# Performance work log

Measured on AMD Instinct MI355X. Metric: run time of the kernel, lower is better.

Reference implementation:

```python
import jax, jax.numpy as jnp
import numpy as np

N = 6000      # residues (nodes)
E = 120000    # edges (~20 neighbors per node)
D = 128       # node_embedding_dim
De = 128      # edge_embedding_dim
H = 4         # attention heads
L = 2         # encoder layers
C = 2 * D + De
NB, BMIN, BMAX = 16, 2.0, 22.0  # RBF params


def _ln(x, g, b):
    m = x.mean(-1, keepdims=True)
    v = ((x - m) ** 2).mean(-1, keepdims=True)
    return (x - m) / jnp.sqrt(v + 1e-5) * g + b


def setup_inputs() -> dict:
    key = jax.random.key(0)
    ks = iter(jax.random.split(key, 64))

    def nrm(shape, scale=0.05):
        return jax.random.normal(next(ks), shape, jnp.float32) * scale

    inp = {}
    inp['sequence_indices'] = jax.random.randint(next(ks), (N,), 0, 21)
    inp['edge_index'] = jax.random.randint(next(ks), (2, E), 0, N)
    inp['edge_distances'] = BMIN + (BMAX - BMIN) * jax.random.uniform(next(ks), (E,), jnp.float32)
    # parameters
    inp['seq_embed'] = nrm((21, D), 1.0)
    inp['edge_lin_W'] = nrm((NB, De)); inp['edge_lin_b'] = jnp.zeros((De,), jnp.float32)
    inp['aW_W'] = nrm((L, H, C, D)); inp['aW_b'] = jnp.zeros((L, H, D), jnp.float32)
    inp['aA_W'] = nrm((L, H, D));    inp['aA_b'] = jnp.zeros((L, H), jnp.float32)
    inp['nmlp_W1'] = nrm((L, C, D)); inp['nmlp_b1'] = jnp.zeros((L, D), jnp.float32)
    inp['nmlp_W2'] = nrm((L, D, D)); inp['nmlp_b2'] = jnp.zeros((L, D), jnp.float32)
    inp['nmlp_W3'] = nrm((L, D, D)); inp['nmlp_b3'] = jnp.zeros((L, D), jnp.float32)
    inp['dmlp_W1'] = nrm((L, D, 4 * D)); inp['dmlp_b1'] = jnp.zeros((L, 4 * D), jnp.float32)
    inp['dmlp_W2'] = nrm((L, 4 * D, D)); inp['dmlp_b2'] = jnp.zeros((L, D), jnp.float32)
    inp['emlp_W1'] = nrm((L, C, De));  inp['emlp_b1'] = jnp.zeros((L, De), jnp.float32)
    inp['emlp_W2'] = nrm((L, De, De)); inp['emlp_b2'] = jnp.zeros((L, De), jnp.float32)
    inp['emlp_W3'] = nrm((L, De, De)); inp['emlp_b3'] = jnp.zeros((L, De), jnp.float32)
    inp['aggr_W'] = nrm((L, H * D, D)); inp['aggr_b'] = jnp.zeros((L, D), jnp.float32)
    inp['n1_g'] = jnp.ones((L, D), jnp.float32);  inp['n1_b'] = jnp.zeros((L, D), jnp.float32)
    inp['e_g'] = jnp.ones((L, De), jnp.float32);  inp['e_b'] = jnp.zeros((L, De), jnp.float32)
    return inp


def reference(sequence_indices, edge_index, edge_distances, seq_embed,
              edge_lin_W, edge_lin_b, aW_W, aW_b, aA_W, aA_b,
              nmlp_W1, nmlp_b1, nmlp_W2, nmlp_b2, nmlp_W3, nmlp_b3,
              dmlp_W1, dmlp_b1, dmlp_W2, dmlp_b2,
              emlp_W1, emlp_b1, emlp_W2, emlp_b2, emlp_W3, emlp_b3,
              aggr_W, aggr_b, n1_g, n1_b, e_g, e_b):
    gelu = lambda x: jax.nn.gelu(x, approximate=False)  # torch default GELU is exact erf
    lrelu = lambda x: jnp.where(x > 0, x, 0.2 * x)      # LeakyReLU(0.2)

    nodes = seq_embed[sequence_indices]                  # [N, D]
    mu = jnp.linspace(BMIN, BMAX, NB)
    sig = (BMAX - BMIN) / NB
    rbf = jnp.exp(-(((edge_distances[:, None] - mu) / sig) ** 2)) + 1e-8  # [E, NB]
    eattr = rbf @ edge_lin_W + edge_lin_b                # [E, De]

    src, snk = edge_index[0], edge_index[1]
    n = nodes.shape[0]
    for l in range(L):
        feat = jnp.concatenate([nodes[src], nodes[snk], eattr], axis=1)        # [E, C]
        h = lrelu(jnp.einsum('ec,hcd->ehd', feat, aW_W[l]) + aW_b[l][None])    # [E, H, D]
        scores = jnp.einsum('ehd,hd->eh', h, aA_W[l]) + aA_b[l][None]          # [E, H]
        nupd = gelu(feat @ nmlp_W1[l] + nmlp_b1[l])
        nupd = gelu(nupd @ nmlp_W2[l] + nmlp_b2[l])
        nupd = nupd @ nmlp_W3[l] + nmlp_b3[l]                                   # [E, D]
        # scatter softmax over sink nodes (per head)
        smax = jax.ops.segment_max(scores, snk, num_segments=n)                 # [N, H]
        att = jnp.exp(scores - smax[snk])                                       # [E, H]
        norm = jax.ops.segment_sum(att + 1e-12, snk, num_segments=n)            # [N, H]
        att = att / norm[snk]
        msg = (att[:, :, None] * nupd[:, None, :]).reshape(E, H * D)            # head-major concat
        agg = jax.ops.segment_sum(msg, snk, num_segments=n)                     # [N, H*D]
        upd = agg @ aggr_W[l] + aggr_b[l]                                       # [N, D]
        nodes = _ln(nodes + upd, n1_g[l], n1_b[l])
        dense = gelu(nodes @ dmlp_W1[l] + dmlp_b1[l]) @ dmlp_W2[l] + dmlp_b2[l]
        # faithful to source: node_norm1 reused, residual re-adds attention update
        nodes = _ln(dense + upd, n1_g[l], n1_b[l])
        ef = jnp.concatenate([nodes[src], nodes[snk], eattr], axis=1)
        eu = gelu(ef @ emlp_W1[l] + emlp_b1[l])
        eu = gelu(eu @ emlp_W2[l] + emlp_b2[l])
        eu = eu @ emlp_W3[l] + emlp_b3[l]
        eattr = _ln(eattr + eu, e_g[l], e_b[l])
    return nodes, eattr
```

## Files before the change

### kernel.cpp

```cpp
#include <hip/hip_runtime.h>
#include <stdint.h>

#define NN 6000
#define EE 120000
#define DD 128
#define CC 384
#define HDIM 512
#define OUT_NODES (NN*DD)
#define OUT_TOTAL (NN*DD + EE*DD)
#define NODE_LO (NN*DD)
#define EDGE_LO (EE*DD)

typedef unsigned short u16;
typedef __bf16 bf16x8 __attribute__((ext_vector_type(8)));
typedef float f32x4 __attribute__((ext_vector_type(4)));

__device__ __forceinline__ float bf2f(u16 u){ union{unsigned i; float f;} x; x.i=(unsigned)u<<16; return x.f; }
__device__ __forceinline__ u16 f2bf(float f){ union{unsigned i; float f;} x; x.f=f; unsigned r=(x.i + 0x7fffu + ((x.i>>16)&1u))>>16; return (u16)r; }
__device__ __forceinline__ float gelu_f(float v){ return 0.5f*v*(1.f + erff(v*0.70710678118654752f)); }

__device__ __forceinline__ void stage16(void* l, const void* g) {
#if __has_builtin(__builtin_amdgcn_global_load_lds)
  __builtin_amdgcn_global_load_lds(
      (__attribute__((address_space(1))) void*)g,
      (__attribute__((address_space(3))) void*)l, 16, 0, 0);
#else
  *(uint4*)l = *(const uint4*)g;
#endif
}

__device__ __forceinline__ void mfma_step(const u16* buf, int wm, int wn, int lane,
                                          f32x4 acc[4][4])
{
  const int ml = lane & 15;
  const int qx = ((lane >> 4) ^ ((ml ^ (ml >> 2)) & 3)) & 3;
  bf16x8 a_h[4], a_l[4], v_h[4], v_l[4];
#pragma unroll
  for (int mi = 0; mi < 4; ++mi) {
    int ro = (wm*64 + mi*16 + ml)*32 + qx*8;
    a_h[mi] = *(const bf16x8*)(buf + ro);
    a_l[mi] = *(const bf16x8*)(buf + 4096 + ro);
  }
#pragma unroll
  for (int ni = 0; ni < 4; ++ni) {
    int ro = (wn*64 + ni*16 + ml)*32 + qx*8;
    v_h[ni] = *(const bf16x8*)(buf + 8192 + ro);
    v_l[ni] = *(const bf16x8*)(buf + 12288 + ro);
  }
#pragma unroll
  for (int mi = 0; mi < 4; ++mi)
#pragma unroll
    for (int ni = 0; ni < 4; ++ni) {
      acc[mi][ni] = __builtin_amdgcn_mfma_f32_16x16x32_bf16(a_h[mi], v_l[ni], acc[mi][ni], 0, 0, 0);
      acc[mi][ni] = __builtin_amdgcn_mfma_f32_16x16x32_bf16(a_l[mi], v_h[ni], acc[mi][ni], 0, 0, 0);
      acc[mi][ni] = __builtin_amdgcn_mfma_f32_16x16x32_bf16(a_h[mi], v_h[ni], acc[mi][ni], 0, 0, 0);
    }
}

__device__ __forceinline__ int xswz(int row, int col) {
  return row*128 + (col ^ ((row&3)<<3) ^ (((row>>2)&3)<<4));
}

__device__ __forceinline__ void mfma_stepX(const u16* X0, const u16* X1, const u16* BB,
                                           int t, int wm, int wn, int lane, f32x4 acc[4][4])
{
  const int ml = lane & 15, qq = lane >> 4;
  const int qx = (qq ^ ((ml ^ (ml >> 2)) & 3)) & 3;
  bf16x8 a_h[4], a_l[4], v_h[4], v_l[4];
#pragma unroll
  for (int mi = 0; mi < 4; ++mi) {
    int o = xswz(wm*64 + mi*16 + ml, t*32 + qq*8);
    a_h[mi] = *(const bf16x8*)(X0 + o);
    a_l[mi] = *(const bf16x8*)(X1 + o);
  }
#pragma unroll
  for (int ni = 0; ni < 4; ++ni) {
    int ro = (wn*64 + ni*16 + ml)*32 + qx*8;
    v_h[ni] = *(const bf16x8*)(BB + ro);
    v_l[ni] = *(const bf16x8*)(BB + 4096 + ro);
  }
#pragma unroll
  for (int mi = 0; mi < 4; ++mi)
#pragma unroll
    for (int ni = 0; ni < 4; ++ni) {
      acc[mi][ni] = __builtin_amdgcn_mfma_f32_16x16x32_bf16(a_h[mi], v_l[ni], acc[mi][ni], 0, 0, 0);
      acc[mi][ni] = __builtin_amdgcn_mfma_f32_16x16x32_bf16(a_l[mi], v_h[ni], acc[mi][ni], 0, 0, 0);
      acc[mi][ni] = __builtin_amdgcn_mfma_f32_16x16x32_bf16(a_h[mi], v_h[ni], acc[mi][ni], 0, 0, 0);
    }
}

__device__ __forceinline__ void coop_loadZ(
    float* ZT, const float* __restrict__ Zg, int zld, int zs0, int zn0,
    const int* __restrict__ src, const int* __restrict__ snk,
    int m0, int M, int tid)
{
#pragma unroll
  for (int it = 0; it < 16; ++it) {
    int idx = it*256 + tid;
    int row = idx >> 5, c4 = idx & 31;
    int gm = m0 + row; if (gm > M-1) gm = M-1;
    const float4 a4 = *((const float4*)(Zg + (size_t)src[gm]*zld + zs0) + c4);
    const float4 b4 = *((const float4*)(Zg + (size_t)snk[gm]*zld + zn0) + c4);
    float4 s4; s4.x = a4.x+b4.x; s4.y = a4.y+b4.y; s4.z = a4.z+b4.z; s4.w = a4.w+b4.w;
    int cs = (c4*4) ^ (((row>>2)&1)<<4);
    *(float4*)(ZT + row*128 + cs) = s4;
  }
}

__device__ __forceinline__ void scatter_X(f32x4 acc[4][4], const float* bias, int gelu_on,
                                          u16* X0, u16* X1, int tid)
{
  const int lane = tid & 63, cl = lane & 15, qr = (lane>>4)&3;
  const int wm = (tid>>6)&1, wn = (tid>>7)&1;
#pragma unroll
  for (int ni = 0; ni < 4; ++ni) {
    float bv = bias[wn*64 + ni*16 + cl];
#pragma unroll
    for (int mi = 0; mi < 4; ++mi)
#pragma unroll
      for (int rg = 0; rg < 4; ++rg) {
        int row = wm*64 + mi*16 + qr*4 + rg;
        int col = wn*64 + ni*16 + cl;
        float v = acc[mi][ni][rg] + bv;
        if (gelu_on) v = gelu_f(v);
        u16 h = f2bf(v);
        int o = xswz(row, col);
        X0[o] = h; X1[o] = f2bf(v - bf2f(h));
      }
  }
}

__device__ __forceinline__ void epilogue_f32(
    f32x4 acc[4][4], const float* bias, float* Cp, int M, int ldc,
    int m0, int n0, int tid)
{
  const int lane = tid & 63;
  const int wm = (tid>>6)&1, wn = (tid>>7)&1;
  const int rl = wm*64 + ((lane>>4)&3)*4;
  const int cl0 = wn*64 + (lane & 15);
#pragma unroll
  for (int ni = 0; ni < 4; ++ni) {
    int gn = n0 + cl0 + ni*16;
    float bv = bias ? bias[gn] : 0.f;
#pragma unroll
    for (int mi = 0; mi < 4; ++mi)
#pragma unroll
      for (int rg = 0; rg < 4; ++rg) {
        int gm = m0 + rl + mi*16 + rg;
        if (gm < M) Cp[(size_t)gm*ldc + gn] = acc[mi][ni][rg] + bv;
      }
  }
}

__device__ __forceinline__ void epilogue_hl(
    f32x4 acc[4][4], const float* bias, u16* Ch, u16* Cl, u16* SM,
    int M, int ldn, int gelu_on, int m0, int n0, int tid)
{
  const int lane = tid & 63, cl = lane & 15, qr = (lane>>4)&3;
  const int wm = (tid>>6)&1, wn = (tid>>7)&1;
#pragma unroll
  for (int ni = 0; ni < 4; ++ni) {
    float bv = bias[n0 + wn*64 + cl + ni*16];
#pragma unroll
    for (int mi = 0; mi < 4; ++mi)
#pragma unroll
      for (int rg = 0; rg < 4; ++rg) {
        float v = acc[mi][ni][rg] + bv;
        if (gelu_on) v = gelu_f(v);
        acc[mi][ni][rg] = v;
      }
  }
#pragma unroll
  for (int pass = 0; pass < 2; ++pass) {
#pragma unroll
    for (int mi = 0; mi < 4; ++mi)
#pragma unroll
      for (int ni = 0; ni < 4; ++ni)
#pragma unroll
        for (int rg = 0; rg < 4; ++rg) {
          int row = wm*64 + mi*16 + qr*4 + rg;
          int col = wn*64 + ni*16 + cl;
          float v = acc[mi][ni][rg];
          u16 h = f2bf(v);
          u16 w = pass ? f2bf(v - bf2f(h)) : h;
          SM[row*128 + (col ^ (qr<<4))] = w;
        }
    __syncthreads();
    u16* Cp = pass ? Cl : Ch;
#pragma unroll
    for (int it = 0; it < 8; ++it) {
      int idx = it*256 + tid;
      int row = idx >> 4, blk = idx & 15;
      uint4 val = *(const uint4*)(SM + row*128 + ((blk*8) ^ (((row>>2)&3)<<4)));
      int gm = m0 + row;
      if (gm < M) *(uint4*)(Cp + (size_t)gm*ldn + n0 + blk*8) = val;
    }
    __syncthreads();
  }
}

__global__ __launch_bounds__(256) void k_gemm2(
    const u16* A_h, const u16* A_l, int K,
    const u16* __restrict__ Bh, const u16* __restrict__ Bl,
    const float* __restrict__ bias, float* Cf,
    u16* Ch, u16* Cl, int M, int ldc, int epi)
{
  __shared__ __align__(16) u16 SM[2][16384];
  const int tid = threadIdx.x, lane = tid & 63;
  const int m0 = blockIdx.x*128, n0 = blockIdx.y*128;
  const int wm = (tid>>6)&1, wn = (tid>>7)&1;
  const u16* gA[2]; const u16* gAl[2]; const u16* gB[2]; const u16* gBl[2];
#pragma unroll
  for (int r = 0; r < 2; ++r) {
    int c = r*256 + tid, m = c>>2, q = c&3;
    int qs = q ^ ((m ^ (m>>2)) & 3);
    int gl = m0 + m; if (gl > M-1) gl = M-1;
    gA[r]  = A_h + (size_t)gl*K + qs*8;
    gAl[r] = A_l + (size_t)gl*K + qs*8;
    gB[r]  = Bh + (size_t)(n0+m)*K + qs*8;
    gBl[r] = Bl + (size_t)(n0+m)*K + qs*8;
  }
  auto stage = [&](int t, u16* buf) {
    int kt = t*32;
#pragma unroll
    for (int r = 0; r < 2; ++r) {
      int c8 = (r*256 + tid)*8;
      stage16(buf + c8,         gA[r]  + kt);
      stage16(buf + 4096 + c8,  gAl[r] + kt);
      stage16(buf + 8192 + c8,  gB[r]  + kt);
      stage16(buf + 12288 + c8, gBl[r] + kt);
    }
  };
  f32x4 acc[4][4] = {};
  const int nk = K >> 5;
  stage(0, SM[0]);
  for (int t = 0; t < nk; ++t) {
    __syncthreads();
    if (t + 1 < nk) stage(t + 1, SM[(t+1)&1]);
    mfma_step(SM[t&1], wm, wn, lane, acc);
  }
  __syncthreads();
  if (epi == 3) epilogue_f32(acc, bias, Cf, M, ldc, m0, n0, tid);
  else          epilogue_hl(acc, bias, Ch, Cl, SM[0], M, ldc, epi == 5, m0, n0, tid);
}

__global__ __launch_bounds__(256) void k_mlp_chain(
    const u16* __restrict__ nodes_h, const u16* __restrict__ eattr_h,
    const int* __restrict__ src, const int* __restrict__ snk,
    const u16* __restrict__ B1h, const u16* __restrict__ B1l, const float* __restrict__ b1,
    const u16* __restrict__ B2h, const u16* __restrict__ B2l, const float* __restrict__ b2,
    const u16* __restrict__ B3h, const u16* __restrict__ B3l, const float* __restrict__ b3,
    u16* __restrict__ Xh, u16* __restrict__ Xl, int M)
{
  __shared__ __align__(16) u16 SM[2][16384];
  __shared__ __align__(16) u16 BB[8192];
  const int tid = threadIdx.x, lane = tid & 63;
  const int m0 = blockIdx.x*128;
  const int wm = (tid>>6)&1, wn = (tid>>7)&1;
  const u16* pr0[2]; const u16* pr1[2]; const u16* pr2[2];
  const u16* gB[2]; const u16* gBl[2];
  int soff[2];
#pragma unroll
  for (int r = 0; r < 2; ++r) {
    int c = r*256 + tid, m = c>>2, q = c&3;
    int qs = q ^ ((m ^ (m>>2)) & 3);
    int gl = m0 + m; if (gl > M-1) gl = M-1;
    pr0[r] = nodes_h + (size_t)src[gl]*DD + qs*8;
    pr1[r] = nodes_h + (size_t)snk[gl]*DD + qs*8;
    pr2[r] = eattr_h + (size_t)gl*DD + qs*8;
    gB[r]  = B1h + (size_t)m*CC + qs*8;
    gBl[r] = B1l + (size_t)m*CC + qs*8;
    soff[r] = m*128 + qs*8;
  }
  auto stage_g = [&](int t, u16* buf) {
    int reg = t >> 2, kk = (t & 3) * 32;
    const int LO = (reg == 2) ? EDGE_LO : NODE_LO;
#pragma unroll
    for (int r = 0; r < 2; ++r) {
      int c8 = (r*256 + tid)*8;
      const u16* g = (reg == 0 ? pr0[r] : reg == 1 ? pr1[r] : pr2[r]) + kk;
      stage16(buf + c8,         g);
      stage16(buf + 4096 + c8,  g + LO);
      stage16(buf + 8192 + c8,  gB[r]  + t*32);
      stage16(buf + 12288 + c8, gBl[r] + t*32);
    }
  };
  auto stageB = [&](const u16* Bh_, const u16* Bl_, int t) {
#pragma unroll
    for (int r = 0; r < 2; ++r) {
      int c8 = (r*256 + tid)*8;
      stage16(BB + c8,        Bh_ + soff[r] + t*32);
      stage16(BB + 4096 + c8, Bl_ + soff[r] + t*32);
    }
  };
  f32x4 acc[4][4] = {};
  stage_g(0, SM[0]);
  for (int t = 0; t < 12; ++t) {
    __syncthreads();
    if (t < 11) stage_g(t + 1, SM[(t+1)&1]);
    mfma_step(SM[t&1], wm, wn, lane, acc);
  }
  __syncthreads();
  scatter_X(acc, b1, 1, (u16*)SM[0], (u16*)SM[1], tid);
  __syncthreads();
#pragma unroll
  for (int mi = 0; mi < 4; ++mi)
#pragma unroll
    for (int ni = 0; ni < 4; ++ni)
#pragma unroll
      for (int rg = 0; rg < 4; ++rg) acc[mi][ni][rg] = 0.f;
  for (int t = 0; t < 4; ++t) {
    stageB(B2h, B2l, t);
    __syncthreads();
    mfma_stepX((const u16*)SM[0], (const u16*)SM[1], BB, t, wm, wn, lane, acc);
    __syncthreads();
  }
  scatter_X(acc, b2, 1, (u16*)SM[0], (u16*)SM[1], tid);
  __syncthreads();
#pragma unroll
  for (int mi = 0; mi < 4; ++mi)
#pragma unroll
    for (int ni = 0; ni < 4; ++ni)
#pragma unroll
      for (int rg = 0; rg < 4; ++rg) acc[mi][ni][rg] = 0.f;
  for (int t = 0; t < 4; ++t) {
    stageB(B3h, B3l, t);
    __syncthreads();
    mfma_stepX((const u16*)SM[0], (const u16*)SM[1], BB, t, wm, wn, lane, acc);
    __syncthreads();
  }
  epilogue_hl(acc, b3, Xh, Xl, (u16*)SM[0], M, 128, 0, m0, 0, tid);
}

__global__ __launch_bounds__(256) void k_score(
    const u16* __restrict__ eattr_h,
    const int* __restrict__ src, const int* __restrict__ snk,
    const u16* __restrict__ Bh, const u16* __restrict__ Bl,
    const float* __restrict__ bias,
    const float* __restrict__ aAw, const float* __restrict__ aAb,
    const float* __restrict__ Zatt,
    float* __restrict__ scores_out, int M)
{
  __shared__ __align__(16) u16 SM[2][16384];
  const int tid = threadIdx.x, lane = tid & 63;
  int p = (blockIdx.x & 7) * 469 + (blockIdx.x >> 3);
  const int bm = p >> 2, bn = p & 3;
  const int m0 = bm*128, n0 = bn*128;
  const int wm = (tid>>6)&1, wn = (tid>>7)&1;
  const u16* pr2[2]; const u16* gB[2]; const u16* gBl[2];
#pragma unroll
  for (int r = 0; r < 2; ++r) {
    int c = r*256 + tid, m = c>>2, q = c&3;
    int qs = q ^ ((m ^ (m>>2)) & 3);
    int gl = m0 + m; if (gl > M-1) gl = M-1;
    pr2[r] = eattr_h + (size_t)gl*DD + qs*8;
    gB[r]  = Bh + (size_t)(n0+m)*DD + qs*8;
    gBl[r] = Bl + (size_t)(n0+m)*DD + qs*8;
  }
  auto stage_s = [&](int t, u16* buf) {
#pragma unroll
    for (int r = 0; r < 2; ++r) {
      int c8 = (r*256 + tid)*8;
      stage16(buf + c8,         pr2[r] + t*32);
      stage16(buf + 4096 + c8,  pr2[r] + EDGE_LO + t*32);
      stage16(buf + 8192 + c8,  gB[r]  + t*32);
      stage16(buf + 12288 + c8, gBl[r] + t*32);
    }
  };
  f32x4 acc[4][4] = {};
  stage_s(0, SM[0]);
  for (int t = 0; t < 4; ++t) {
    __syncthreads();
    if (t < 3) stage_s(t + 1, SM[(t+1)&1]);
    mfma_step(SM[t&1], wm, wn, lane, acc);
  }
  __syncthreads();
  float* ZT = (float*)SM;
  coop_loadZ(ZT, Zatt, 1024, n0, 512 + n0, src, snk, m0, M, tid);
  __syncthreads();
  const int cl = lane & 15, qr = (lane>>4)&3;
  float pv[16];
#pragma unroll
  for (int mi = 0; mi < 4; ++mi)
#pragma unroll
    for (int rg = 0; rg < 4; ++rg) {
      int row = wm*64 + mi*16 + qr*4 + rg;
      int s = ((row>>2)&1)<<4;
      float pacc = 0.f;
#pragma unroll
      for (int ni = 0; ni < 4; ++ni) {
        int lc = wn*64 + ni*16 + cl;
        int gn = n0 + lc;
        float v = acc[mi][ni][rg] + bias[gn] + ZT[row*128 + (lc ^ s)];
        v = (v > 0.f) ? v : 0.2f*v;
        pacc += v * aAw[gn];
      }
      pacc += __shfl_xor(pacc, 1, 64); pacc += __shfl_xor(pacc, 2, 64);
      pacc += __shfl_xor(pacc, 4, 64); pacc += __shfl_xor(pacc, 8, 64);
      pv[mi*4 + rg] = pacc;
    }
  __syncthreads();
  float* sred = (float*)SM[0];
#pragma unroll
  for (int mi = 0; mi < 4; ++mi)
#pragma unroll
    for (int rg = 0; rg < 4; ++rg)
      if (cl == 0) sred[wn*128 + wm*64 + mi*16 + qr*4 + rg] = pv[mi*4 + rg];
  __syncthreads();
  if (tid < 128) {
    int gm = m0 + tid;
    if (gm < M) scores_out[(size_t)gm*4 + bn] = sred[tid] + sred[128 + tid] + aAb[bn];
  }
}

__global__ void k_detect(const u16* __restrict__ d, int n, int* __restrict__ flag) {
  __shared__ int cnt;
  if (threadIdx.x == 0) cnt = 0;
  __syncthreads();
  int c = 0;
  for (int i = threadIdx.x; i < n; i += blockDim.x) {
    int e = (d[i] >> 7) & 0xff;
    if (e >= 0xC0) ++c;
  }
  atomicAdd(&cnt, c);
  __syncthreads();
  if (threadIdx.x == 0) *flag = (cnt > 16) ? 1 : 0;
}

struct ConvDesc { const void* src; float* dst; int n; };
struct ConvArgs { ConvDesc d[30]; };
__global__ void k_conv32(ConvArgs a, const int* __restrict__ flag) {
  ConvDesc de = a.d[blockIdx.y];
  int fp = *flag;
  for (int i = blockIdx.x*256 + threadIdx.x; i < de.n; i += gridDim.x*256)
    de.dst[i] = fp ? ((const float*)de.src)[i] : bf2f(((const u16*)de.src)[i]);
}

struct PackDesc { const float* src; u16* dh; u16* dl; int K, N, sk, sh; };
struct PackArgs { PackDesc d[32]; int n; };
__global__ void k_pack2(PackArgs a) {
  PackDesc de = a.d[blockIdx.y];
  int total = de.K * de.N;
  for (int i = blockIdx.x*256 + threadIdx.x; i < total; i += gridDim.x*256) {
    int k = i / de.N, n = i - k*de.N;
    float x = de.src[(size_t)k*de.sk + (n & 127) + (n >> 7)*de.sh];
    u16 h = f2bf(x);
    de.dh[(size_t)n*de.K + k] = h;
    de.dl[(size_t)n*de.K + k] = f2bf(x - bf2f(h));
  }
}

__global__ void k_init_nodes(const int* __restrict__ seq, const float* __restrict__ emb,
                             float* __restrict__ nodes_f, u16* __restrict__ nh) {
  int i = blockIdx.x*256 + threadIdx.x;
  if (i >= NN*DD) return;
  int n = i >> 7, d = i & 127;
  float v = emb[seq[n]*DD + d];
  nodes_f[i] = v;
  u16 h = f2bf(v); nh[i] = h; nh[NODE_LO + i] = f2bf(v - bf2f(h));
}

__global__ void k_rbf_s(const float* __restrict__ dist, const float* __restrict__ W,
                        const float* __restrict__ b, u16* __restrict__ eh) {
  int e = blockIdx.x, t = threadIdx.x;
  float d = dist[e];
  float acc = b[t];
#pragma unroll
  for (int k = 0; k < 16; ++k) {
    float mu = 2.f + (20.f/15.f)*(float)k;
    float z = (d - mu)*0.8f;
    float r = expf(-z*z) + 1e-8f;
    acc += r*W[k*DD + t];
  }
  size_t idx = (size_t)e*DD + t;
  u16 h = f2bf(acc); eh[idx] = h; eh[(size_t)EDGE_LO + idx] = f2bf(acc - bf2f(h));
}

__global__ void k_hist(const int* __restrict__ snk, int* __restrict__ deg) {
  int e = blockIdx.x*256 + threadIdx.x;
  if (e < EE) atomicAdd(&deg[snk[e]], 1);
}
__global__ void k_scan(const int* __restrict__ deg, int* __restrict__ ptr, int* __restrict__ cursor, int n) {
  __shared__ int buf[1024];
  __shared__ int carry_s;
  int tid = threadIdx.x;
  if (tid == 0) carry_s = 0;
  __syncthreads();
  for (int base = 0; base < n; base += 1024) {
    int i = base + tid;
    int v = (i < n) ? deg[i] : 0;
    buf[tid] = v;
    __syncthreads();
    for (int off = 1; off < 1024; off <<= 1) {
      int t = (tid >= off) ? buf[tid - off] : 0;
      __syncthreads();
      buf[tid] += t;
      __syncthreads();
    }
    int excl = buf[tid] - v;
    int carry = carry_s;
    if (i < n) { ptr[i] = carry + excl; cursor[i] = carry + excl; }
    __syncthreads();
    if (tid == 1023) carry_s = carry + buf[1023];
    __syncthreads();
  }
  if (tid == 0) ptr[n] = carry_s;
}
__global__ void k_scatter(const int* __restrict__ snk, int* __restrict__ cursor, int* __restrict__ csr) {
  int e = blockIdx.x*256 + threadIdx.x;
  if (e < EE) { int p = atomicAdd(&cursor[snk[e]], 1); csr[p] = e; }
}

__global__ void k_softmax(const float* __restrict__ scores, const int* __restrict__ ptr,
                          const int* __restrict__ csr, float* __restrict__ att, int nnodes) {
  int node = blockIdx.x*4 + (threadIdx.x >> 6);
  if (node >= nnodes) return;
  int lane = threadIdx.x & 63;
  int h = lane >> 4, j = lane & 15;
  int b = ptr[node], e = ptr[node+1];
  float mx = -1e30f;
  for (int i = b + j; i < e; i += 16) mx = fmaxf(mx, scores[(size_t)csr[i]*4 + h]);
  mx = fmaxf(mx, __shfl_xor(mx, 1, 64)); mx = fmaxf(mx, __shfl_xor(mx, 2, 64));
  mx = fmaxf(mx, __shfl_xor(mx, 4, 64)); mx = fmaxf(mx, __shfl_xor(mx, 8, 64));
  float s = 0.f;
  for (int i = b + j; i < e; i += 16) s += expf(scores[(size_t)csr[i]*4 + h] - mx);
  s += __shfl_xor(s, 1, 64); s += __shfl_xor(s, 2, 64);
  s += __shfl_xor(s, 4, 64); s += __shfl_xor(s, 8, 64);
  float norm = s + (float)(e - b)*1e-12f;
  float inv = (e > b) ? 1.f/norm : 0.f;
  for (int i = b + j; i < e; i += 16) {
    int ed = csr[i];
    att[(size_t)ed*4 + h] = expf(scores[(size_t)ed*4 + h] - mx)*inv;
  }
}

__global__ void k_aggregate(const float* __restrict__ att,
                            const u16* __restrict__ Xh, const u16* __restrict__ Xl,
                            const int* __restrict__ ptr, const int* __restrict__ csr,
                            u16* __restrict__ agg_h, u16* __restrict__ agg_l) {
  int node = blockIdx.x; int d = threadIdx.x;
  int b = ptr[node], e = ptr[node+1];
  float a0=0.f, a1=0.f, a2=0.f, a3=0.f;
  for (int i = b; i < e; ++i) {
    int ed = csr[i];
    float4 a = *(const float4*)(att + (size_t)ed*4);
    size_t xo = (size_t)ed*DD + d;
    float v = bf2f(Xh[xo]) + bf2f(Xl[xo]);
    a0 += a.x*v; a1 += a.y*v; a2 += a.z*v; a3 += a.w*v;
  }
  size_t o = (size_t)node*HDIM + d;
  float vv[4] = {a0, a1, a2, a3};
#pragma unroll
  for (int h = 0; h < 4; ++h) {
    u16 hi = f2bf(vv[h]);
    agg_h[o + h*128] = hi;
    agg_l[o + h*128] = f2bf(vv[h] - bf2f(hi));
  }
}

__global__ void k_ln_node(float* __restrict__ nodes_f,
                          const float* __restrict__ upd, const float* __restrict__ dense_f,
                          const float* __restrict__ g, const float* __restrict__ b,
                          int mode, int rows, u16* __restrict__ nh) {
  int r = blockIdx.x*4 + (threadIdx.x >> 6);
  if (r >= rows) return;
  int lane = threadIdx.x & 63;
  size_t o = (size_t)r*DD;
  float x0, x1;
  if (mode == 0) { x0 = nodes_f[o+lane]; x1 = nodes_f[o+lane+64]; }
  else           { x0 = dense_f[o+lane]; x1 = dense_f[o+lane+64]; }
  x0 += upd[o+lane]; x1 += upd[o+lane+64];
  float s = x0 + x1;
#pragma unroll
  for (int m = 1; m < 64; m <<= 1) s += __shfl_xor(s, m, 64);
  float mean = s * (1.f/128.f);
  float d0 = x0 - mean, d1 = x1 - mean;
  float vv = d0*d0 + d1*d1;
#pragma unroll
  for (int m = 1; m < 64; m <<= 1) vv += __shfl_xor(vv, m, 64);
  float inv = rsqrtf(vv*(1.f/128.f) + 1e-5f);
  float v0 = d0*inv*g[lane]    + b[lane];
  float v1 = d1*inv*g[lane+64] + b[lane+64];
  nodes_f[o+lane]    = v0;
  nodes_f[o+lane+64] = v1;
  u16 h0 = f2bf(v0), h1 = f2bf(v1);
  nh[o+lane] = h0;    nh[NODE_LO + o+lane]    = f2bf(v0 - bf2f(h0));
  nh[o+lane+64] = h1; nh[NODE_LO + o+lane+64] = f2bf(v1 - bf2f(h1));
}

__global__ void k_ln_edge(const u16* __restrict__ Xh, const u16* __restrict__ Xl,
                          const float* __restrict__ g, const float* __restrict__ b,
                          int rows, u16* __restrict__ eh) {
  int r = blockIdx.x*4 + (threadIdx.x >> 6);
  if (r >= rows) return;
  int lane = threadIdx.x & 63;
  size_t o = (size_t)r*DD;
  float x0 = bf2f(eh[o+lane])    + bf2f(eh[(size_t)EDGE_LO + o+lane])
           + bf2f(Xh[o+lane])    + bf2f(Xl[o+lane]);
  float x1 = bf2f(eh[o+lane+64]) + bf2f(eh[(size_t)EDGE_LO + o+lane+64])
           + bf2f(Xh[o+lane+64]) + bf2f(Xl[o+lane+64]);
  float s = x0 + x1;
#pragma unroll
  for (int m = 1; m < 64; m <<= 1) s += __shfl_xor(s, m, 64);
  float mean = s * (1.f/128.f);
  float d0 = x0 - mean, d1 = x1 - mean;
  float vv = d0*d0 + d1*d1;
#pragma unroll
  for (int m = 1; m < 64; m <<= 1) vv += __shfl_xor(vv, m, 64);
  float inv = rsqrtf(vv*(1.f/128.f) + 1e-5f);
  float v0 = d0*inv*g[lane]    + b[lane];
  float v1 = d1*inv*g[lane+64] + b[lane+64];
  u16 h0 = f2bf(v0), h1 = f2bf(v1);
  eh[o+lane] = h0;    eh[(size_t)EDGE_LO + o+lane]    = f2bf(v0 - bf2f(h0));
  eh[o+lane+64] = h1; eh[(size_t)EDGE_LO + o+lane+64] = f2bf(v1 - bf2f(h1));
}

__global__ void k_finalize(const float* __restrict__ nodes_f, const u16* __restrict__ eh,
                           void* __restrict__ out, const int* __restrict__ flag) {
  int i = blockIdx.x*256 + threadIdx.x;
  if (i >= OUT_TOTAL) return;
  int fp = *flag;
  float v;
  if (i < OUT_NODES) v = nodes_f[i];
  else { int j = i - OUT_NODES; v = bf2f(eh[j]) + bf2f(eh[(size_t)EDGE_LO + j]); }
  if (fp) ((float*)out)[i] = v; else ((u16*)out)[i] = f2bf(v);
}

extern "C" void kernel_launch(void* const* d_in, const int* in_sizes, int n_in,
                              void* d_out, int out_size, void* d_ws, size_t ws_size,
                              hipStream_t stream)
{
  const int* seq_idx = (const int*)d_in[0];
  const int* esrc = (const int*)d_in[1];
  const int* esnk = ((const int*)d_in[1]) + EE;

  char* wsp = (char*)d_ws;
  size_t off = 0;
  auto carve = [&](size_t bytes)->char* {
    char* p = wsp + off; off += (bytes + 255) & ~(size_t)255; return p;
  };
  int* flag       = (int*)carve(256);
  float* nodes_f  = (float*)carve((size_t)NN*DD*4);
  float* upd_f    = (float*)carve((size_t)NN*DD*4);
  float* scores   = (float*)carve((size_t)EE*4*4);
  float* att      = (float*)carve((size_t)EE*4*4);
  float* dense_f  = (float*)carve((size_t)NN*DD*4);
  float* Zatt     = (float*)carve((size_t)NN*1024*4);
  u16* wpk_h      = (u16*)carve(557056ULL*2*2);
  u16* wpk_l      = (u16*)carve(557056ULL*2*2);
  int* deg        = (int*)carve((size_t)NN*4);
  int* ptrb       = (int*)carve((size_t)(NN+1)*4);
  int* cursor     = (int*)carve((size_t)NN*4);
  int* csr        = (int*)carve((size_t)EE*4);
  u16* nodes_h    = (u16*)carve((size_t)2*NN*DD*2);
  u16* eattr_h    = (u16*)carve((size_t)2*EE*DD*2);
  u16* X_h        = (u16*)carve((size_t)2*EE*DD*2);
  u16* agg_h      = (u16*)carve((size_t)2*NN*HDIM*2);
  u16* dh_h       = (u16*)carve((size_t)2*NN*HDIM*2);
  u16* X_l   = X_h   + (size_t)EE*DD;
  u16* agg_l = agg_h + (size_t)NN*HDIM;
  u16* dh_l  = dh_h  + (size_t)NN*HDIM;

  static const int FCNT[32] = {0,0,120000,2688,2048,128,393216,1024,1024,8,
    98304,256,32768,256,32768,256, 131072,1024,131072,256,
    98304,256,32768,256,32768,256, 131072,256, 256,256,256,256};
  float* cf[32];
  for (int i = 2; i < 32; ++i) cf[i] = (float*)carve((size_t)FCNT[i]*4);
  (void)ws_size; (void)in_sizes; (void)n_in; (void)out_size;

  k_detect<<<1, 1024, 0, stream>>>((const u16*)d_in[2], 120000, flag);
  ConvArgs ca;
  for (int i = 2; i < 32; ++i) { ca.d[i-2].src = d_in[i]; ca.d[i-2].dst = cf[i]; ca.d[i-2].n = FCNT[i]; }
  hipLaunchKernelGGL(k_conv32, dim3(96, 30), dim3(256), 0, stream, ca, flag);

  const size_t PW_L = 557056;
  PackArgs pa; int nd = 0;
  for (int l = 0; l < 2; ++l) {
    size_t base = l*PW_L;
    auto add = [&](const float* s, size_t doff, int K, int N, int sk, int sh){
      pa.d[nd].src = s; pa.d[nd].dh = wpk_h + doff; pa.d[nd].dl = wpk_l + doff;
      pa.d[nd].K = K; pa.d[nd].N = N; pa.d[nd].sk = sk; pa.d[nd].sh = sh; ++nd; };
    const float* aW = cf[6] + l*196608;
    add(aW,          base + 0,      128, 512, 128, 49152);
    add(aW + 16384,  base + 65536,  128, 512, 128, 49152);
    add(aW + 32768,  base + 131072, 128, 512, 128, 49152);
    add(cf[10] + l*49152, base + 196608, 384, 128, 128, 0);
    add(cf[12] + l*16384, base + 245760, 128, 128, 128, 0);
    add(cf[14] + l*16384, base + 262144, 128, 128, 128, 0);
    add(cf[26] + l*65536, base + 278528, 512, 128, 128, 0);
    add(cf[16] + l*65536, base + 344064, 128, 512, 512, 128);
    add(cf[18] + l*65536, base + 409600, 512, 128, 128, 0);
    add(cf[20] + l*49152, base + 475136, 384, 128, 128, 0);
    add(cf[22] + l*16384, base + 524288, 128, 128, 128, 0);
    add(cf[24] + l*16384, base + 540672, 128, 128, 128, 0);
  }
  pa.n = nd;
  hipLaunchKernelGGL(k_pack2, dim3(256, nd), dim3(256), 0, stream, pa);

  k_init_nodes<<<(NN*DD + 255)/256, 256, 0, stream>>>(seq_idx, cf[3], nodes_f, nodes_h);
  k_rbf_s<<<EE, 128, 0, stream>>>(cf[2], cf[4], cf[5], eattr_h);

  (void)hipMemsetAsync(deg, 0, (size_t)NN*4, stream);
  k_hist<<<(EE + 255)/256, 256, 0, stream>>>(esnk, deg);
  k_scan<<<1, 1024, 0, stream>>>(deg, ptrb, cursor, NN);
  k_scatter<<<(EE + 255)/256, 256, 0, stream>>>(esnk, cursor, csr);

  for (int l = 0; l < 2; ++l) {
    const u16* bh = wpk_h + l*PW_L; const u16* bl = wpk_l + l*PW_L;
    k_gemm2<<<dim3(47, 8), 256, 0, stream>>>(nodes_h, nodes_h + NODE_LO, 128,
        bh + 0, bl + 0, nullptr, Zatt, nullptr, nullptr, NN, 1024, 3);
    k_score<<<dim3(3752), 256, 0, stream>>>(eattr_h, esrc, esnk,
        bh + 131072, bl + 131072, cf[7] + l*512, cf[8] + l*512, cf[9] + l*4,
        Zatt, scores, EE);
    k_mlp_chain<<<dim3(938), 256, 0, stream>>>(nodes_h, eattr_h, esrc, esnk,
        bh + 196608, bl + 196608, cf[11] + l*128,
        bh + 245760, bl + 245760, cf[13] + l*128,
        bh + 262144, bl + 262144, cf[15] + l*128,
        X_h, X_l, EE);
    k_softmax<<<(NN + 3)/4, 256, 0, stream>>>(scores, ptrb, csr, att, NN);
    k_aggregate<<<NN, 128, 0, stream>>>(att, X_h, X_l, ptrb, csr, agg_h, agg_l);
    k_gemm2<<<dim3(47, 1), 256, 0, stream>>>(agg_h, agg_l, 512, bh + 278528, bl + 278528,
        cf[27] + l*128, upd_f, nullptr, nullptr, NN, 128, 3);
    k_ln_node<<<(NN + 3)/4, 256, 0, stream>>>(nodes_f, upd_f, (const float*)nullptr,
        cf[28] + l*128, cf[29] + l*128, 0, NN, nodes_h);
    k_gemm2<<<dim3(47, 4), 256, 0, stream>>>(nodes_h, nodes_h + NODE_LO, 128,
        bh + 344064, bl + 344064, cf[17] + l*512, nullptr, dh_h, dh_l, NN, 512, 5);
    k_gemm2<<<dim3(47, 1), 256, 0, stream>>>(dh_h, dh_l, 512, bh + 409600, bl + 409600,
        cf[19] + l*128, dense_f, nullptr, nullptr, NN, 128, 3);
    k_ln_node<<<(NN + 3)/4, 256, 0, stream>>>(nodes_f, upd_f, dense_f,
        cf[28] + l*128, cf[29] + l*128, 1, NN, nodes_h);
    k_mlp_chain<<<dim3(938), 256, 0, stream>>>(nodes_h, eattr_h, esrc, esnk,
        bh + 475136, bl + 475136, cf[21] + l*128,
        bh + 524288, bl + 524288, cf[23] + l*128,
        bh + 540672, bl + 540672, cf[25] + l*128,
        X_h, X_l, EE);
    k_ln_edge<<<(EE + 3)/4, 256, 0, stream>>>(X_h, X_l,
        cf[30] + l*128, cf[31] + l*128, EE, eattr_h);
  }
  k_finalize<<<(OUT_TOTAL + 255)/256, 256, 0, stream>>>(nodes_f, eattr_h, d_out, flag);
}
```

Baseline: 1.367 ms.

## Store Zatt in bf16 and process score edges in CSR sink order

The per-node attention projection Zatt is now written as a single bf16 array with a new LDS-staged epilogue instead of fp32, which halves the gathered bytes in the score kernel. The score kernel also walks edges in CSR (sink-sorted) order, so neighbouring rows share sink nodes and their Zatt gathers hit cache more often. Scores are scattered back to the original edge index. In exchange, eattr rows are now gathered indirectly, and Zatt loses precision: it drops the hi/lo split and is truncated to one bf16 term, which may affect accuracy.

Measured after the change: 1.175 ms. 14.1% less time.

```diff
diff --git a/kernel.cpp b/kernel.cpp
--- a/kernel.cpp
+++ b/kernel.cpp
@@ -15,6 +15,8 @@
 typedef __bf16 bf16x8 __attribute__((ext_vector_type(8)));
 typedef float f32x4 __attribute__((ext_vector_type(4)));
 
+union V8 { u16 s[8]; uint4 v; };
+
 __device__ __forceinline__ float bf2f(u16 u){ union{unsigned i; float f;} x; x.i=(unsigned)u<<16; return x.f; }
 __device__ __forceinline__ u16 f2bf(float f){ union{unsigned i; float f;} x; x.f=f; unsigned r=(x.i + 0x7fffu + ((x.i>>16)&1u))>>16; return (u16)r; }
 __device__ __forceinline__ float gelu_f(float v){ return 0.5f*v*(1.f + erff(v*0.70710678118654752f)); }
@@ -89,21 +91,24 @@
     }
 }
 
-__device__ __forceinline__ void coop_loadZ(
-    float* ZT, const float* __restrict__ Zg, int zld, int zs0, int zn0,
+__device__ __forceinline__ void coop_loadZ_b(
+    float* ZT, const u16* __restrict__ Zh, int zld, int zs0, int zn0,
     const int* __restrict__ src, const int* __restrict__ snk,
-    int m0, int M, int tid)
-{
-#pragma unroll
-  for (int it = 0; it < 16; ++it) {
+    const int* __restrict__ csr, int m0, int M, int tid)
+{
+#pragma unroll
+  for (int it = 0; it < 8; ++it) {
     int idx = it*256 + tid;
-    int row = idx >> 5, c4 = idx & 31;
+    int row = idx >> 4, c8 = idx & 15;
     int gm = m0 + row; if (gm > M-1) gm = M-1;
-    const float4 a4 = *((const float4*)(Zg + (size_t)src[gm]*zld + zs0) + c4);
-    const float4 b4 = *((const float4*)(Zg + (size_t)snk[gm]*zld + zn0) + c4);
-    float4 s4; s4.x = a4.x+b4.x; s4.y = a4.y+b4.y; s4.z = a4.z+b4.z; s4.w = a4.w+b4.w;
-    int cs = (c4*4) ^ (((row>>2)&1)<<4);
-    *(float4*)(ZT + row*128 + cs) = s4;
+    int e = csr[gm];
+    V8 a8, b8;
+    a8.v = *(const uint4*)(Zh + (size_t)src[e]*zld + zs0 + c8*8);
+    b8.v = *(const uint4*)(Zh + (size_t)snk[e]*zld + zn0 + c8*8);
+    int base = (c8*8) ^ (((row>>2)&1)<<4);
+    float* d = ZT + row*128 + base;
+#pragma unroll
+    for (int j = 0; j < 8; ++j) d[j] = bf2f(a8.s[j]) + bf2f(b8.s[j]);
   }
 }
 
@@ -152,6 +157,33 @@
   }
 }
 
+__device__ __forceinline__ void epilogue_h1(
+    f32x4 acc[4][4], u16* Cp, u16* SM, int M, int ldn, int m0, int n0, int tid)
+{
+  const int lane = tid & 63, cl = lane & 15, qr = (lane>>4)&3;
+  const int wm = (tid>>6)&1, wn = (tid>>7)&1;
+#pragma unroll
+  for (int mi = 0; mi < 4; ++mi)
+#pragma unroll
+    for (int ni = 0; ni < 4; ++ni)
+#pragma unroll
+      for (int rg = 0; rg < 4; ++rg) {
+        int row = wm*64 + mi*16 + qr*4 + rg;
+        int col = wn*64 + ni*16 + cl;
+        SM[row*128 + (col ^ (qr<<4))] = f2bf(acc[mi][ni][rg]);
+      }
+  __syncthreads();
+#pragma unroll
+  for (int it = 0; it < 8; ++it) {
+    int idx = it*256 + tid;
+    int row = idx >> 4, blk = idx & 15;
+    uint4 val = *(const uint4*)(SM + row*128 + ((blk*8) ^ (((row>>2)&3)<<4)));
+    int gm = m0 + row;
+    if (gm < M) *(uint4*)(Cp + (size_t)gm*ldn + n0 + blk*8) = val;
+  }
+  __syncthreads();
+}
+
 __device__ __forceinline__ void epilogue_hl(
     f32x4 acc[4][4], const float* bias, u16* Ch, u16* Cl, u16* SM,
     int M, int ldn, int gelu_on, int m0, int n0, int tid)
@@ -240,8 +272,9 @@
     mfma_step(SM[t&1], wm, wn, lane, acc);
   }
   __syncthreads();
-  if (epi == 3) epilogue_f32(acc, bias, Cf, M, ldc, m0, n0, tid);
-  else          epilogue_hl(acc, bias, Ch, Cl, SM[0], M, ldc, epi == 5, m0, n0, tid);
+  if (epi == 3)      epilogue_f32(acc, bias, Cf, M, ldc, m0, n0, tid);
+  else if (epi == 8) epilogue_h1(acc, Ch, SM[0], M, ldc, m0, n0, tid);
+  else               epilogue_hl(acc, bias, Ch, Cl, SM[0], M, ldc, epi == 5, m0, n0, tid);
 }
 
 __global__ __launch_bounds__(256) void k_mlp_chain(
@@ -335,10 +368,11 @@
 __global__ __launch_bounds__(256) void k_score(
     const u16* __restrict__ eattr_h,
     const int* __restrict__ src, const int* __restrict__ snk,
+    const int* __restrict__ csr,
     const u16* __restrict__ Bh, const u16* __restrict__ Bl,
     const float* __restrict__ bias,
     const float* __restrict__ aAw, const float* __restrict__ aAb,
-    const float* __restrict__ Zatt,
+    const u16* __restrict__ Zatt,
     float* __restrict__ scores_out, int M)
 {
   __shared__ __align__(16) u16 SM[2][16384];
@@ -353,7 +387,8 @@
     int c = r*256 + tid, m = c>>2, q = c&3;
     int qs = q ^ ((m ^ (m>>2)) & 3);
     int gl = m0 + m; if (gl > M-1) gl = M-1;
-    pr2[r] = eattr_h + (size_t)gl*DD + qs*8;
+    int ce = csr[gl];
+    pr2[r] = eattr_h + (size_t)ce*DD + qs*8;
     gB[r]  = Bh + (size_t)(n0+m)*DD + qs*8;
     gBl[r] = Bl + (size_t)(n0+m)*DD + qs*8;
   }
@@ -376,7 +411,7 @@
   }
   __syncthreads();
   float* ZT = (float*)SM;
-  coop_loadZ(ZT, Zatt, 1024, n0, 512 + n0, src, snk, m0, M, tid);
+  coop_loadZ_b(ZT, Zatt, 1024, n0, 512 + n0, src, snk, csr, m0, M, tid);
   __syncthreads();
   const int cl = lane & 15, qr = (lane>>4)&3;
   float pv[16];
@@ -409,7 +444,7 @@
   __syncthreads();
   if (tid < 128) {
     int gm = m0 + tid;
-    if (gm < M) scores_out[(size_t)gm*4 + bn] = sred[tid] + sred[128 + tid] + aAb[bn];
+    if (gm < M) scores_out[(size_t)csr[gm]*4 + bn] = sred[tid] + sred[128 + tid] + aAb[bn];
   }
 }
 
@@ -645,7 +680,7 @@
   float* scores   = (float*)carve((size_t)EE*4*4);
   float* att      = (float*)carve((size_t)EE*4*4);
   float* dense_f  = (float*)carve((size_t)NN*DD*4);
-  float* Zatt     = (float*)carve((size_t)NN*1024*4);
+  u16* Zatt       = (u16*)carve((size_t)NN*1024*2);
   u16* wpk_h      = (u16*)carve(557056ULL*2*2);
   u16* wpk_l      = (u16*)carve(557056ULL*2*2);
   int* deg        = (int*)carve((size_t)NN*4);
@@ -708,8 +743,8 @@
   for (int l = 0; l < 2; ++l) {
     const u16* bh = wpk_h + l*PW_L; const u16* bl = wpk_l + l*PW_L;
     k_gemm2<<<dim3(47, 8), 256, 0, stream>>>(nodes_h, nodes_h + NODE_LO, 128,
-        bh + 0, bl + 0, nullptr, Zatt, nullptr, nullptr, NN, 1024, 3);
-    k_score<<<dim3(3752), 256, 0, stream>>>(eattr_h, esrc, esnk,
+        bh + 0, bl + 0, nullptr, nullptr, Zatt, nullptr, NN, 1024, 8);
+    k_score<<<dim3(3752), 256, 0, stream>>>(eattr_h, esrc, esnk, csr,
         bh + 131072, bl + 131072, cf[7] + l*512, cf[8] + l*512, cf[9] + l*4,
         Zatt, scores, EE);
     k_mlp_chain<<<dim3(938), 256, 0, stream>>>(nodes_h, eattr_h, esrc, esnk,
```
